# Optimization experiments

Hardware: AMD Instinct MI355X
Metric: run time of the kernel (lower is better)

## Reference

```python
import jax, jax.numpy as jnp
import numpy as np

B_SZ, T, D_MODEL, D_STATE, D_CONV = 8, 2048, 768, 16, 4


def setup_inputs() -> dict:
    key = jax.random.key(0)
    ks = jax.random.split(key, 8)
    s = lambda k, shape: (jax.random.normal(k, shape, jnp.float32) * 0.02)
    x = jax.random.normal(ks[0], (B_SZ, T, D_MODEL), jnp.float32)
    # A_log initialized as log(arange(1, d_state+1)) broadcast over d_model
    A_log = jnp.log(jnp.broadcast_to(jnp.arange(1, D_STATE + 1, dtype=jnp.float32), (D_MODEL, D_STATE)))
    return {
        "x": x,
        "W_in": s(ks[1], (2 * D_MODEL, D_MODEL)),          # in_proj (no bias)
        "conv_w": s(ks[2], (D_MODEL, 1, D_CONV)),          # depthwise conv kernel (O, I/groups, K)
        "conv_b": jnp.zeros((D_MODEL,), jnp.float32),
        "W_dt": s(ks[3], (D_MODEL, D_MODEL)),              # dt_proj weight
        "b_dt": jnp.zeros((D_MODEL,), jnp.float32),
        "A_log": A_log,
        "D_param": jnp.ones((D_MODEL,), jnp.float32),
        "W_B": s(ks[4], (D_STATE, D_MODEL)),               # B_proj (no bias)
        "W_C": s(ks[5], (D_STATE, D_MODEL)),               # C_proj (no bias)
    }


def reference(x, W_in, conv_w, conv_b, W_dt, b_dt, A_log, D_param, W_B, W_C):
    B_, T_, D = x.shape
    N = A_log.shape[1]
    K = conv_w.shape[-1]

    xz = x @ W_in.T                                # [B, T, 2D]
    x_ssm = xz[..., :D]                            # z = xz[..., D:] is unused in the original forward

    # depthwise causal conv: torch pads both sides K-1 then slices to T == left-pad K-1
    xc = jnp.transpose(x_ssm, (0, 2, 1))           # [B, D, T]
    xc = jax.lax.conv_general_dilated(xc, conv_w, (1,), [(K - 1, 0)], feature_group_count=D)
    xc = xc + conv_b[None, :, None]
    x_conv = jax.nn.silu(jnp.transpose(xc, (0, 2, 1)))  # [B, T, D]

    dt = jax.nn.softplus(x_conv @ W_dt.T + b_dt)   # [B, T, D]
    A = -jnp.exp(A_log)                            # [D, N]
    Bm = x_conv @ W_B.T                            # [B, T, N]
    Cm = x_conv @ W_C.T                            # [B, T, N]

    def step(h, inp):
        dt_t, B_t, C_t, x_t = inp                  # [B,D], [B,N], [B,N], [B,D]
        dA = jnp.exp(A[None] * dt_t[:, :, None])   # [B, D, N]
        h = h * dA + x_t[:, :, None] * (dt_t[:, :, None] * B_t[:, None, :])
        y_t = jnp.einsum('bdn,bn->bd', h, C_t)
        return h, y_t

    h0 = jnp.zeros((B_, D, N), x.dtype)
    inps = (jnp.swapaxes(dt, 0, 1), jnp.swapaxes(Bm, 0, 1),
            jnp.swapaxes(Cm, 0, 1), jnp.swapaxes(x, 0, 1))
    _, ys = jax.lax.scan(step, h0, inps)           # ys: [T, B, D]
    y = jnp.swapaxes(ys, 0, 1)                     # [B, T, D]
    return y + x * D_param[None, None, :]
```

## Files before the change

kernel.cpp:

```cpp
#include <hip/hip_runtime.h>
#include <hip/hip_bf16.h>
#include <cstdint>

#define D_MODELX 768
#define D_STATEX 16
#define TSEQ 2048
#define BSZ 8
#define KCONV 4

typedef unsigned short ushort_t;
typedef __attribute__((ext_vector_type(8))) short short8v;
typedef __attribute__((ext_vector_type(4))) float floatx4;

__device__ __forceinline__ unsigned short f2bf(float f) {
  unsigned int u = __float_as_uint(f);
  unsigned int r = u + 0x7FFFu + ((u >> 16) & 1u);
  return (unsigned short)(r >> 16);
}
__device__ __forceinline__ float bf2f(unsigned short s) {
  return __uint_as_float(((unsigned int)s) << 16);
}
__device__ __forceinline__ float softplus_f(float v) {
  return fmaxf(v, 0.f) + log1pf(expf(-fabsf(v)));
}
__device__ __forceinline__ void gload_lds16(const void* gsrc, void* ldst) {
  __builtin_amdgcn_global_load_lds(
      (const __attribute__((address_space(1))) unsigned int*)gsrc,
      (__attribute__((address_space(3))) unsigned int*)ldst, 16, 0, 0);
}

__global__ __launch_bounds__(256) void split_hl(
    const float* __restrict__ in, ushort_t* __restrict__ hi,
    ushort_t* __restrict__ lo, int n4)
{
  int i = blockIdx.x * 256 + threadIdx.x;
  if (i >= n4) return;
  float4 v = ((const float4*)in)[i];
  ushort4 h, l;
  ushort_t hb;
  hb = f2bf(v.x); h.x = hb; l.x = f2bf(v.x - bf2f(hb));
  hb = f2bf(v.y); h.y = hb; l.y = f2bf(v.y - bf2f(hb));
  hb = f2bf(v.z); h.z = hb; l.z = f2bf(v.z - bf2f(hb));
  hb = f2bf(v.w); h.w = hb; l.w = f2bf(v.w - bf2f(hb));
  ((ushort4*)hi)[i] = h;
  ((ushort4*)lo)[i] = l;
}

#define GBM 128
#define GBN 128
#define GBK 32

__global__ __launch_bounds__(256) void gemm_bf16x3(
    const ushort_t* __restrict__ Ah, const ushort_t* __restrict__ Al,
    const ushort_t* __restrict__ Wh, const ushort_t* __restrict__ Wl,
    float* __restrict__ C, int M, int N, int K,
    const float* __restrict__ bias, int epi)
{
  __shared__ ushort_t lds[4 * 4096];
  const int tid = threadIdx.x;
  const int wid = tid >> 6;
  const int lane = tid & 63;
  const int row0 = blockIdx.y * GBM;
  const int col0 = blockIdx.x * GBN;

  const ushort_t* gbase = (wid == 0) ? Ah : (wid == 1) ? Al : (wid == 2) ? Wh : Wl;
  const int gr0 = (wid < 2) ? row0 : col0;
  ushort_t* lt = &lds[wid * 4096];

  const int wr = wid >> 1, wc = wid & 1;
  const int frow = lane & 15;
  const int kb = lane >> 4;
  const int abase = kb * 1024 + (wr * 64 + frow) * 8;
  const int bbase = kb * 1024 + (wc * 64 + frow) * 8;

  floatx4 acc[4][4];
  #pragma unroll
  for (int i = 0; i < 4; ++i)
    #pragma unroll
    for (int j = 0; j < 4; ++j) acc[i][j] = (floatx4){0.f, 0.f, 0.f, 0.f};

  for (int kt = 0; kt < K; kt += GBK) {
    const ushort_t* gk = gbase + (size_t)gr0 * K + kt;
    #pragma unroll
    for (int i = 0; i < 8; ++i) {
      const int kbs = i >> 1, mh = i & 1;
      gload_lds16(gk + (size_t)(mh * 64 + lane) * K + kbs * 8,
                  lt + kbs * 1024 + mh * 512);
    }
    __syncthreads();

    short8v ah[4], al[4], bh[4], bl[4];
    #pragma unroll
    for (int mi = 0; mi < 4; ++mi) {
      ah[mi] = *(const short8v*)&lds[0 * 4096 + abase + mi * 128];
      al[mi] = *(const short8v*)&lds[1 * 4096 + abase + mi * 128];
    }
    #pragma unroll
    for (int nj = 0; nj < 4; ++nj) {
      bh[nj] = *(const short8v*)&lds[2 * 4096 + bbase + nj * 128];
      bl[nj] = *(const short8v*)&lds[3 * 4096 + bbase + nj * 128];
    }
    #pragma unroll
    for (int mi = 0; mi < 4; ++mi)
      #pragma unroll
      for (int nj = 0; nj < 4; ++nj) {
        acc[mi][nj] = __builtin_amdgcn_mfma_f32_16x16x32_bf16(ah[mi], bh[nj], acc[mi][nj], 0, 0, 0);
        acc[mi][nj] = __builtin_amdgcn_mfma_f32_16x16x32_bf16(ah[mi], bl[nj], acc[mi][nj], 0, 0, 0);
        acc[mi][nj] = __builtin_amdgcn_mfma_f32_16x16x32_bf16(al[mi], bh[nj], acc[mi][nj], 0, 0, 0);
      }
    __syncthreads();
  }

  const int rbase = row0 + wr * 64 + (lane >> 4) * 4;
  #pragma unroll
  for (int nj = 0; nj < 4; ++nj) {
    const int col = col0 + wc * 64 + nj * 16 + frow;
    const float bcol = (epi == 1) ? bias[col] : 0.f;
    #pragma unroll
    for (int mi = 0; mi < 4; ++mi) {
      #pragma unroll
      for (int r = 0; r < 4; ++r) {
        float v = acc[mi][nj][r];
        if (epi == 1) v = softplus_f(v + bcol);
        C[(size_t)(rbase + mi * 16 + r) * N + col] = v;
      }
    }
  }
}

__global__ __launch_bounds__(256) void conv_silu_k(
    const float* __restrict__ xs, const float* __restrict__ w,
    const float* __restrict__ bias, ushort_t* __restrict__ oh, ushort_t* __restrict__ ol)
{
  int idx = blockIdx.x * blockDim.x + threadIdx.x;
  const int D4 = D_MODELX / 4;
  int d4 = idx % D4, bt = idx / D4;
  int t = bt & (TSEQ - 1);
  int d = d4 * 4;

  float wv[4][4];
  #pragma unroll
  for (int i = 0; i < 4; ++i) *(float4*)wv[i] = *(const float4*)(w + (d + i) * KCONV);

  float accv[4];
  *(float4*)accv = *(const float4*)(bias + d);

  #pragma unroll
  for (int j = 0; j < KCONV; ++j) {
    int off = KCONV - 1 - j;
    if (t >= off) {
      float xv[4];
      *(float4*)xv = *(const float4*)(xs + (size_t)(bt - off) * D_MODELX + d);
      #pragma unroll
      for (int i = 0; i < 4; ++i) accv[i] = fmaf(xv[i], wv[i][j], accv[i]);
    }
  }
  ushort4 h, l;
  ushort_t hb;
  float s0 = accv[0] / (1.f + expf(-accv[0]));
  float s1 = accv[1] / (1.f + expf(-accv[1]));
  float s2 = accv[2] / (1.f + expf(-accv[2]));
  float s3 = accv[3] / (1.f + expf(-accv[3]));
  hb = f2bf(s0); h.x = hb; l.x = f2bf(s0 - bf2f(hb));
  hb = f2bf(s1); h.y = hb; l.y = f2bf(s1 - bf2f(hb));
  hb = f2bf(s2); h.z = hb; l.z = f2bf(s2 - bf2f(hb));
  hb = f2bf(s3); h.w = hb; l.w = f2bf(s3 - bf2f(hb));
  const size_t o4 = ((size_t)bt * D_MODELX + d) >> 2;
  ((ushort4*)oh)[o4] = h;
  ((ushort4*)ol)[o4] = l;
}

__global__ __launch_bounds__(256) void bc_gemm(
    const ushort_t* __restrict__ xh, const ushort_t* __restrict__ xl,
    const float* __restrict__ WB, const float* __restrict__ WC,
    float* __restrict__ Bm, float* __restrict__ Cm, int K)
{
  const int tid = threadIdx.x;
  const int col = tid & 31;
  const int r = tid >> 5;
  const int row = blockIdx.x * 8 + r;
  const float* wrow = (col < 16) ? (WB + (size_t)col * K) : (WC + (size_t)(col - 16) * K);
  const ushort_t* xhr = xh + (size_t)row * K;
  const ushort_t* xlr = xl + (size_t)row * K;
  float s = 0.f;
  for (int k = 0; k < K; k += 4) {
    ushort4 hv = *(const ushort4*)(xhr + k);
    ushort4 lv = *(const ushort4*)(xlr + k);
    float4 wv = *(const float4*)(wrow + k);
    s = fmaf(bf2f(hv.x) + bf2f(lv.x), wv.x, s);
    s = fmaf(bf2f(hv.y) + bf2f(lv.y), wv.y, s);
    s = fmaf(bf2f(hv.z) + bf2f(lv.z), wv.z, s);
    s = fmaf(bf2f(hv.w) + bf2f(lv.w), wv.w, s);
  }
  if (col < 16) Bm[(size_t)row * 16 + col] = s;
  else          Cm[(size_t)row * 16 + (col - 16)] = s;
}

#define NSEG 32
#define LSEG 64
#define NSTATE (BSZ * D_MODELX * D_STATEX)

__global__ __launch_bounds__(256) void scan_phase1(
    const float* __restrict__ x, const float* __restrict__ dt,
    const float* __restrict__ Bm, const float* __restrict__ A_log,
    float* __restrict__ P, float* __restrict__ Q)
{
  __shared__ float dt_s[LSEG][16], x_s[LSEG][16], B_s[LSEG][16];
  const int tiles_per_b = D_MODELX / 16;
  const int bid = blockIdx.x;
  const int dtile = bid % tiles_per_b;
  const int seg = (bid / tiles_per_b) % NSEG;
  const int b = bid / (tiles_per_b * NSEG);
  const int d0 = dtile * 16;
  const int tid = threadIdx.x;
  const int n = tid & 15, dd = tid >> 4;
  const int d = d0 + dd;

  const float A_dn = -__expf(A_log[d * D_STATEX + n]);

  const int ltt = tid >> 2;
  const int lc4 = (tid & 3) * 4;
  {
    const int t = seg * LSEG + ltt;
    const size_t base = ((size_t)b * TSEQ + t) * D_MODELX + d0 + lc4;
    const size_t bbase = ((size_t)b * TSEQ + t) * D_STATEX + lc4;
    *(float4*)&dt_s[ltt][lc4] = *(const float4*)(dt + base);
    *(float4*)&x_s[ltt][lc4]  = *(const float4*)(x + base);
    *(float4*)&B_s[ltt][lc4]  = *(const float4*)(Bm + bbase);
  }
  __syncthreads();

  float h = 0.f, Pp = 1.f;
  #pragma unroll 8
  for (int tt = 0; tt < LSEG; ++tt) {
    float dtv = dt_s[tt][dd];
    float xv  = x_s[tt][dd];
    float bv  = B_s[tt][n];
    float a   = __expf(A_dn * dtv);
    Pp *= a;
    h = fmaf(h, a, xv * dtv * bv);
  }
  const size_t g = ((size_t)b * D_MODELX + d0) * D_STATEX + tid;
  P[(size_t)seg * NSTATE + g] = Pp;
  Q[(size_t)seg * NSTATE + g] = h;
}

__global__ __launch_bounds__(256) void scan_combine(
    float* __restrict__ P, float* __restrict__ Q)
{
  const size_t g = (size_t)blockIdx.x * 256 + threadIdx.x;
  float H = 0.f;
  #pragma unroll
  for (int s = 0; s < NSEG; ++s) {
    float p = P[(size_t)s * NSTATE + g];
    float q = Q[(size_t)s * NSTATE + g];
    P[(size_t)s * NSTATE + g] = H;
    H = fmaf(p, H, q);
  }
}

__global__ __launch_bounds__(256) void scan_phase2(
    const float* __restrict__ x, const float* __restrict__ dt,
    const float* __restrict__ Bm, const float* __restrict__ Cm,
    const float* __restrict__ A_log, const float* __restrict__ Dp,
    const float* __restrict__ Hinit, float* __restrict__ y)
{
  __shared__ float dt_s[LSEG][16], x_s[LSEG][16], B_s[LSEG][16], C_s[LSEG][16], y_s[LSEG][16];
  const int tiles_per_b = D_MODELX / 16;
  const int bid = blockIdx.x;
  const int dtile = bid % tiles_per_b;
  const int seg = (bid / tiles_per_b) % NSEG;
  const int b = bid / (tiles_per_b * NSEG);
  const int d0 = dtile * 16;
  const int tid = threadIdx.x;
  const int n = tid & 15, dd = tid >> 4;
  const int d = d0 + dd;

  const float A_dn = -__expf(A_log[d * D_STATEX + n]);
  const size_t g = ((size_t)b * D_MODELX + d0) * D_STATEX + tid;
  float h = Hinit[(size_t)seg * NSTATE + g];

  const int ltt = tid >> 2;
  const int lc4 = (tid & 3) * 4;
  float dv[4];
  *(float4*)dv = *(const float4*)(Dp + d0 + lc4);

  const int t = seg * LSEG + ltt;
  const size_t base = ((size_t)b * TSEQ + t) * D_MODELX + d0 + lc4;
  {
    const size_t bbase = ((size_t)b * TSEQ + t) * D_STATEX + lc4;
    *(float4*)&dt_s[ltt][lc4] = *(const float4*)(dt + base);
    *(float4*)&x_s[ltt][lc4]  = *(const float4*)(x + base);
    *(float4*)&B_s[ltt][lc4]  = *(const float4*)(Bm + bbase);
    *(float4*)&C_s[ltt][lc4]  = *(const float4*)(Cm + bbase);
  }
  __syncthreads();

  #pragma unroll 4
  for (int tt = 0; tt < LSEG; ++tt) {
    float dtv = dt_s[tt][dd];
    float xv  = x_s[tt][dd];
    float bv  = B_s[tt][n];
    float cv  = C_s[tt][n];
    float a   = __expf(A_dn * dtv);
    h = fmaf(h, a, xv * dtv * bv);
    float p = h * cv;
    p += __shfl_xor(p, 1);
    p += __shfl_xor(p, 2);
    p += __shfl_xor(p, 4);
    p += __shfl_xor(p, 8);
    if (n == 0) y_s[tt][dd] = p;
  }
  __syncthreads();

  float yv[4], xv[4];
  *(float4*)yv = *(const float4*)&y_s[ltt][lc4];
  *(float4*)xv = *(const float4*)&x_s[ltt][lc4];
  #pragma unroll
  for (int i = 0; i < 4; ++i) yv[i] = fmaf(xv[i], dv[i], yv[i]);
  *(float4*)(y + base) = *(const float4*)yv;
}

extern "C" void kernel_launch(void* const* d_in, const int* in_sizes, int n_in,
                              void* d_out, int out_size, void* d_ws, size_t ws_size,
                              hipStream_t stream) {
  const float* x      = (const float*)d_in[0];
  const float* W_in   = (const float*)d_in[1];
  const float* conv_w = (const float*)d_in[2];
  const float* conv_b = (const float*)d_in[3];
  const float* W_dt   = (const float*)d_in[4];
  const float* b_dt   = (const float*)d_in[5];
  const float* A_log  = (const float*)d_in[6];
  const float* D_par  = (const float*)d_in[7];
  const float* W_B    = (const float*)d_in[8];
  const float* W_C    = (const float*)d_in[9];
  float* y = (float*)d_out;

  const int M = BSZ * TSEQ;
  const size_t MD = (size_t)M * D_MODELX;
  const size_t WD = (size_t)D_MODELX * D_MODELX;

  char* p = (char*)d_ws;
  float* x_ssm = (float*)p;       p += MD * 4;
  ushort_t* xh = (ushort_t*)p;
  ushort_t* xl = xh + MD;         p += MD * 2 * 2;
  ushort_t* Wh_in = (ushort_t*)p; p += WD * 2;
  ushort_t* Wl_in = (ushort_t*)p; p += WD * 2;
  ushort_t* Wh_dt = (ushort_t*)p; p += WD * 2;
  ushort_t* Wl_dt = (ushort_t*)p; p += WD * 2;
  float* Bm = (float*)p;          p += (size_t)M * D_STATEX * 4;
  float* Cm = (float*)p;          p += (size_t)M * D_STATEX * 4;

  split_hl<<<(int)(MD / 4 / 256), 256, 0, stream>>>(x, xh, xl, (int)(MD / 4));
  split_hl<<<(int)(WD / 4 / 256), 256, 0, stream>>>(W_in, Wh_in, Wl_in, (int)(WD / 4));
  split_hl<<<(int)(WD / 4 / 256), 256, 0, stream>>>(W_dt, Wh_dt, Wl_dt, (int)(WD / 4));

  gemm_bf16x3<<<dim3(D_MODELX / GBN, M / GBM), 256, 0, stream>>>(
      xh, xl, Wh_in, Wl_in, x_ssm, M, D_MODELX, D_MODELX, nullptr, 0);

  ushort_t* xch = xh;
  ushort_t* xcl = xl;
  conv_silu_k<<<(int)(M * (D_MODELX / 4)) / 256, 256, 0, stream>>>(
      x_ssm, conv_w, conv_b, xch, xcl);

  float* dtb = x_ssm;
  gemm_bf16x3<<<dim3(D_MODELX / GBN, M / GBM), 256, 0, stream>>>(
      xch, xcl, Wh_dt, Wl_dt, dtb, M, D_MODELX, D_MODELX, b_dt, 1);

  bc_gemm<<<M / 8, 256, 0, stream>>>(xch, xcl, W_B, W_C, Bm, Cm, D_MODELX);

  float* P = (float*)xh;
  float* Q = P + (size_t)NSEG * NSTATE;
  const int nblk = BSZ * (D_MODELX / 16) * NSEG;
  scan_phase1<<<nblk, 256, 0, stream>>>(x, dtb, Bm, A_log, P, Q);
  scan_combine<<<NSTATE / 256, 256, 0, stream>>>(P, Q);
  scan_phase2<<<nblk, 256, 0, stream>>>(x, dtb, Bm, Cm, A_log, D_par, P, y);
}
```

Baseline: 1.027 ms.

## Fuse B/C projections into dt GEMM via concatenated padded weight matrix

Concatenates W_dt, W_B and W_C (zero-padded to 896 rows) into one split bf16 weight and runs a single MFMA GEMM that writes softplus dt, Bm and Cm from a column-dependent epilogue. This removes the separate scalar bc_gemm kernel, which re-read the whole x_conv hi/lo activations. The cost is one extra 128-column tile per row block, of which 96 columns are zero padding doing wasted MFMA work, plus branchy epilogue stores.

```diff
diff --git a/kernel.cpp b/kernel.cpp
--- a/kernel.cpp
+++ b/kernel.cpp
@@ -7,6 +7,7 @@
 #define TSEQ 2048
 #define BSZ 8
 #define KCONV 4
+#define NCAT 896
 
 typedef unsigned short ushort_t;
 typedef __attribute__((ext_vector_type(8))) short short8v;
@@ -46,6 +47,29 @@
   ((ushort4*)lo)[i] = l;
 }
 
+__global__ __launch_bounds__(256) void split_cat(
+    const float* __restrict__ Wdt, const float* __restrict__ WB,
+    const float* __restrict__ WC, ushort_t* __restrict__ hi, ushort_t* __restrict__ lo)
+{
+  int i = blockIdx.x * 256 + threadIdx.x;
+  if (i >= NCAT * D_MODELX / 4) return;
+  const int row = i / (D_MODELX / 4);
+  const int c = (i % (D_MODELX / 4)) * 4;
+  float4 v;
+  if (row < 768)       v = *(const float4*)(Wdt + (size_t)row * D_MODELX + c);
+  else if (row < 784)  v = *(const float4*)(WB + (size_t)(row - 768) * D_MODELX + c);
+  else if (row < 800)  v = *(const float4*)(WC + (size_t)(row - 784) * D_MODELX + c);
+  else                 v = make_float4(0.f, 0.f, 0.f, 0.f);
+  ushort4 h, l;
+  ushort_t hb;
+  hb = f2bf(v.x); h.x = hb; l.x = f2bf(v.x - bf2f(hb));
+  hb = f2bf(v.y); h.y = hb; l.y = f2bf(v.y - bf2f(hb));
+  hb = f2bf(v.z); h.z = hb; l.z = f2bf(v.z - bf2f(hb));
+  hb = f2bf(v.w); h.w = hb; l.w = f2bf(v.w - bf2f(hb));
+  ((ushort4*)hi)[i] = h;
+  ((ushort4*)lo)[i] = l;
+}
+
 #define GBM 128
 #define GBN 128
 #define GBK 32
@@ -54,7 +78,8 @@
     const ushort_t* __restrict__ Ah, const ushort_t* __restrict__ Al,
     const ushort_t* __restrict__ Wh, const ushort_t* __restrict__ Wl,
     float* __restrict__ C, int M, int N, int K,
-    const float* __restrict__ bias, int epi)
+    const float* __restrict__ bias, int epi,
+    float* __restrict__ Bm, float* __restrict__ Cm)
 {
   __shared__ ushort_t lds[4 * 4096];
   const int tid = threadIdx.x;
@@ -112,17 +137,31 @@
   }
 
   const int rbase = row0 + wr * 64 + (lane >> 4) * 4;
-  #pragma unroll
-  for (int nj = 0; nj < 4; ++nj) {
-    const int col = col0 + wc * 64 + nj * 16 + frow;
-    const float bcol = (epi == 1) ? bias[col] : 0.f;
-    #pragma unroll
-    for (int mi = 0; mi < 4; ++mi) {
+  if (epi == 0) {
+    #pragma unroll
+    for (int nj = 0; nj < 4; ++nj) {
+      const int col = col0 + wc * 64 + nj * 16 + frow;
       #pragma unroll
-      for (int r = 0; r < 4; ++r) {
-        float v = acc[mi][nj][r];
-        if (epi == 1) v = softplus_f(v + bcol);
-        C[(size_t)(rbase + mi * 16 + r) * N + col] = v;
+      for (int mi = 0; mi < 4; ++mi)
+        #pragma unroll
+        for (int r = 0; r < 4; ++r)
+          C[(size_t)(rbase + mi * 16 + r) * N + col] = acc[mi][nj][r];
+    }
+  } else {
+    #pragma unroll
+    for (int nj = 0; nj < 4; ++nj) {
+      const int col = col0 + wc * 64 + nj * 16 + frow;
+      const float bcol = (col < 768) ? bias[col] : 0.f;
+      #pragma unroll
+      for (int mi = 0; mi < 4; ++mi) {
+        #pragma unroll
+        for (int r = 0; r < 4; ++r) {
+          const int row = rbase + mi * 16 + r;
+          const float v = acc[mi][nj][r];
+          if (col < 768)      C[(size_t)row * N + col] = softplus_f(v + bcol);
+          else if (col < 784) Bm[(size_t)row * D_STATEX + (col - 768)] = v;
+          else if (col < 800) Cm[(size_t)row * D_STATEX + (col - 784)] = v;
+        }
       }
     }
   }
@@ -168,32 +207,6 @@
   const size_t o4 = ((size_t)bt * D_MODELX + d) >> 2;
   ((ushort4*)oh)[o4] = h;
   ((ushort4*)ol)[o4] = l;
-}
-
-__global__ __launch_bounds__(256) void bc_gemm(
-    const ushort_t* __restrict__ xh, const ushort_t* __restrict__ xl,
-    const float* __restrict__ WB, const float* __restrict__ WC,
-    float* __restrict__ Bm, float* __restrict__ Cm, int K)
-{
-  const int tid = threadIdx.x;
-  const int col = tid & 31;
-  const int r = tid >> 5;
-  const int row = blockIdx.x * 8 + r;
-  const float* wrow = (col < 16) ? (WB + (size_t)col * K) : (WC + (size_t)(col - 16) * K);
-  const ushort_t* xhr = xh + (size_t)row * K;
-  const ushort_t* xlr = xl + (size_t)row * K;
-  float s = 0.f;
-  for (int k = 0; k < K; k += 4) {
-    ushort4 hv = *(const ushort4*)(xhr + k);
-    ushort4 lv = *(const ushort4*)(xlr + k);
-    float4 wv = *(const float4*)(wrow + k);
-    s = fmaf(bf2f(hv.x) + bf2f(lv.x), wv.x, s);
-    s = fmaf(bf2f(hv.y) + bf2f(lv.y), wv.y, s);
-    s = fmaf(bf2f(hv.z) + bf2f(lv.z), wv.z, s);
-    s = fmaf(bf2f(hv.w) + bf2f(lv.w), wv.w, s);
-  }
-  if (col < 16) Bm[(size_t)row * 16 + col] = s;
-  else          Cm[(size_t)row * 16 + (col - 16)] = s;
 }
 
 #define NSEG 32
@@ -339,6 +352,7 @@
   const int M = BSZ * TSEQ;
   const size_t MD = (size_t)M * D_MODELX;
   const size_t WD = (size_t)D_MODELX * D_MODELX;
+  const size_t WCAT = (size_t)NCAT * D_MODELX;
 
   char* p = (char*)d_ws;
   float* x_ssm = (float*)p;       p += MD * 4;
@@ -346,17 +360,17 @@
   ushort_t* xl = xh + MD;         p += MD * 2 * 2;
   ushort_t* Wh_in = (ushort_t*)p; p += WD * 2;
   ushort_t* Wl_in = (ushort_t*)p; p += WD * 2;
-  ushort_t* Wh_dt = (ushort_t*)p; p += WD * 2;
-  ushort_t* Wl_dt = (ushort_t*)p; p += WD * 2;
+  ushort_t* Wh_ct = (ushort_t*)p; p += WCAT * 2;
+  ushort_t* Wl_ct = (ushort_t*)p; p += WCAT * 2;
   float* Bm = (float*)p;          p += (size_t)M * D_STATEX * 4;
   float* Cm = (float*)p;          p += (size_t)M * D_STATEX * 4;
 
   split_hl<<<(int)(MD / 4 / 256), 256, 0, stream>>>(x, xh, xl, (int)(MD / 4));
   split_hl<<<(int)(WD / 4 / 256), 256, 0, stream>>>(W_in, Wh_in, Wl_in, (int)(WD / 4));
-  split_hl<<<(int)(WD / 4 / 256), 256, 0, stream>>>(W_dt, Wh_dt, Wl_dt, (int)(WD / 4));
+  split_cat<<<(int)((WCAT / 4 + 255) / 256), 256, 0, stream>>>(W_dt, W_B, W_C, Wh_ct, Wl_ct);
 
   gemm_bf16x3<<<dim3(D_MODELX / GBN, M / GBM), 256, 0, stream>>>(
-      xh, xl, Wh_in, Wl_in, x_ssm, M, D_MODELX, D_MODELX, nullptr, 0);
+      xh, xl, Wh_in, Wl_in, x_ssm, M, D_MODELX, D_MODELX, nullptr, 0, nullptr, nullptr);
 
   ushort_t* xch = xh;
   ushort_t* xcl = xl;
@@ -364,10 +378,8 @@
       x_ssm, conv_w, conv_b, xch, xcl);
 
   float* dtb = x_ssm;
-  gemm_bf16x3<<<dim3(D_MODELX / GBN, M / GBM), 256, 0, stream>>>(
-      xch, xcl, Wh_dt, Wl_dt, dtb, M, D_MODELX, D_MODELX, b_dt, 1);
-
-  bc_gemm<<<M / 8, 256, 0, stream>>>(xch, xcl, W_B, W_C, Bm, Cm, D_MODELX);
+  gemm_bf16x3<<<dim3(NCAT / GBN, M / GBM), 256, 0, stream>>>(
+      xch, xcl, Wh_ct, Wl_ct, dtb, M, D_MODELX, D_MODELX, b_dt, 2, Bm, Cm);
 
   float* P = (float*)xh;
   float* Q = P + (size_t)NSEG * NSTATE;
```

Result: faster. 828.1 us (-19.3%).
